# Kernel tuning notes

Hardware: AMD Instinct MI355X
Metric: run time of the kernel (lower is better)

## Reference

```python
import jax, jax.numpy as jnp
import numpy as np

B, F, N, E, T = 8, 16, 1024, 256, 64
ALPHA = 0.2        # LeakyReLU negative slope
NEG = -9.0e15      # masking value used by the torch code


def setup_inputs() -> dict:
    key = jax.random.key(0)
    ks = jax.random.split(key, 9)
    x = jax.random.normal(ks[0], (B, F, N, T), dtype=jnp.float32)
    mask = (jax.random.uniform(ks[1], (B, F, N, T)) > 0.2).astype(jnp.float32)
    # binary incidence matrix [n_nodes, n_edges]; guarantee every hyperedge
    # has at least one incident node (avoids div-by-zero / empty softmax)
    inc = (jax.random.uniform(ks[2], (N, E)) < 0.05).astype(jnp.float32)
    inc = inc.at[0, :].set(1.0)
    h0 = jax.random.normal(ks[3], (1, N), dtype=jnp.float32)      # initial node state row
    h1 = jax.random.normal(ks[4], (E, 1), dtype=jnp.float32)      # initial edge state
    bias = jax.random.uniform(ks[5], (N,), dtype=jnp.float32)     # THGAT.bias (d_model == N)
    weight = jax.random.uniform(ks[6], (2 * F + 1,), dtype=jnp.float32)  # [3*d_in-ish, 1] proj
    weight2 = jax.random.uniform(ks[7], (E, E), dtype=jnp.float32) / E   # edge mixing
    a = jax.random.uniform(ks[8], (2,), dtype=jnp.float32)        # GAT attention vector
    return {"x": x, "mask": mask, "incidence": inc, "h0": h0, "h1": h1,
            "bias": bias, "weight": weight, "weight2": weight2, "a": a}


def _thgat_step(x_s, m_s, n_s, h_e, incidence, bias, weight, weight2, a):
    # x_s, m_s: [B,F,N]; n_s: [B,1,N]; h_e: [B,E,1]
    x_cat = jnp.concatenate([x_s, m_s, n_s], axis=1)          # [B,2F+1,N]
    xn = jnp.einsum('bcn,c->bn', x_cat, weight) + bias         # node feature (scalar per node)
    deg = jnp.sum(incidence, axis=0)                           # [E] hyperedge degree
    edge = (xn @ incidence) / deg                              # [B,E] mean of incident nodes
    edge = edge @ weight2                                      # [B,E]
    # pairwise GAT score at nonzero (n,e) pairs; computed densely then masked,
    # identical math to torch's gather -> sparse_coo -> to_dense path
    s = jax.nn.leaky_relu(xn[:, :, None] * a[0] + edge[:, None, :] * a[1], ALPHA)  # [B,N,E]
    time_e = h_e[:, :, 0] + edge                               # agg_type='sum': pri_e + edge
    s = s + time_e[:, None, :]
    att = jnp.where(incidence[None] > 0, s, NEG)
    attn = jax.nn.softmax(att, axis=1)                         # softmax over nodes per edge
    node = jnp.einsum('bne,be->bn', attn, edge)                # aggregate edge feats to nodes
    return node[:, None, :], edge[:, :, None]                  # [B,1,N], [B,E,1]


def reference(x, mask, incidence, h0, h1, bias, weight, weight2, a):
    n0 = jnp.broadcast_to(h0[None], (B, 1, N))
    e0 = jnp.broadcast_to(h1[None], (B, E, 1))
    xs = jnp.moveaxis(x, -1, 0)     # [T,B,F,N]
    ms = jnp.moveaxis(mask, -1, 0)

    def step(carry, inp):
        n_s, h_e = carry
        x_s, m_s = inp
        node, edge = _thgat_step(x_s, m_s, n_s, h_e, incidence, bias, weight, weight2, a)
        return (node, edge), node[:, 0, :]

    _, nodes = jax.lax.scan(step, (n0, e0), (xs, ms))
    return jnp.moveaxis(nodes, 0, 1)  # [B,T,N] imputations per timestep
```

## Files before the change

### kernel.cpp

```cpp
#include <hip/hip_runtime.h>

#define Bq 8
#define Fq 16
#define Nq 1024
#define Eq 256
#define Tq 64
constexpr float ALPHAq = 0.2f;
constexpr float LOG2Eq = 1.4426950408889634f;
constexpr int NNZCAP = 32768;
constexpr int MAXJE  = 20;
constexpr int NNZW2  = 20480;
constexpr int DUMP0  = NNZW2;
constexpr int WVLTOT = NNZW2 + 1024;

__device__ __forceinline__ float fast_exp2(float x) {
  return __builtin_amdgcn_exp2f(x);
}

__device__ __forceinline__ float qswap1(float x) {
  return __int_as_float(__builtin_amdgcn_mov_dpp(__float_as_int(x), 0xB1, 0xF, 0xF, true));
}
__device__ __forceinline__ float qswap2(float x) {
  return __int_as_float(__builtin_amdgcn_mov_dpp(__float_as_int(x), 0x4E, 0xF, 0xF, true));
}

__global__ __launch_bounds__(256) void k_cntB(const float* __restrict__ inc,
                                              int* __restrict__ gcnt,
                                              int* __restrict__ ncnt) {
  const int i = blockIdx.x, e = threadIdx.x;
  const int base = i * 64;
  int c = 0;
  for (int r = 0; r < 64; ++r) c += (inc[(size_t)(base + r) * Eq + e] > 0.f) ? 1 : 0;
  gcnt[i * Eq + e] = c;
  if (i < 4) {
    const int n = i * 256 + e;
    const float* row = inc + (size_t)n * Eq;
    int cn = 0;
    for (int k = 0; k < Eq; ++k) cn += (row[k] > 0.f) ? 1 : 0;
    ncnt[n] = cn;
  }
}

__global__ __launch_bounds__(1024) void k_prefB(const int* __restrict__ gcnt,
                                                const int* __restrict__ ncnt,
                                                int* __restrict__ g_ptr,
                                                int* __restrict__ goff,
                                                int* __restrict__ tlp,
                                                int* __restrict__ tlp2) {
  __shared__ int tot[Eq];
  __shared__ int sptr[Eq + 1];
  __shared__ int sn[Nq];
  __shared__ int snp[Nq + 1];
  __shared__ int snp2[Nq + 1];
  const int tid = threadIdx.x;
  if (tid < Eq) { int s = 0; for (int i = 0; i < 16; ++i) s += gcnt[i * Eq + tid]; tot[tid] = s; }
  sn[tid] = ncnt[tid];
  __syncthreads();
  if (tid == 0) { int s = 0; for (int j = 0; j < Eq; ++j) { sptr[j] = s; s += tot[j]; } sptr[Eq] = s; }
  if (tid == 1) { int s = 0; for (int i = 0; i < Nq; ++i) { snp[i] = s; s += sn[i]; } snp[Nq] = s; }
  if (tid == 2) { int s = 0; for (int i = 0; i < Nq; ++i) { snp2[i] = s; s += (sn[i] + 3) & ~3; } snp2[Nq] = s; }
  __syncthreads();
  if (tid <= Eq) g_ptr[tid] = sptr[tid];
  tlp[tid] = snp[tid];
  tlp2[tid] = snp2[tid];
  if (tid == 0) { tlp[Nq] = snp[Nq]; tlp2[Nq] = snp2[Nq]; }
  if (tid < Eq) {
    int run = sptr[tid];
    for (int i = 0; i < 16; ++i) { goff[i * Eq + tid] = run; run += gcnt[i * Eq + tid]; }
  }
}

__global__ __launch_bounds__(256) void k_fillB(const float* __restrict__ inc,
                                               const int* __restrict__ goff,
                                               const int* __restrict__ tlp,
                                               unsigned short* __restrict__ g_nodes,
                                               unsigned short* __restrict__ tle_g) {
  const int i = blockIdx.x, e = threadIdx.x;
  const int base = i * 64;
  int w = goff[i * Eq + e];
  for (int r = 0; r < 64; ++r) {
    const int n = base + r;
    if (inc[(size_t)n * Eq + e] > 0.f) { if (w < NNZCAP) g_nodes[w] = (unsigned short)n; ++w; }
  }
  if (i < 4) {
    const int n = i * 256 + e;
    const float* row = inc + (size_t)n * Eq;
    int wn = tlp[n];
    for (int k = 0; k < Eq; ++k)
      if (row[k] > 0.f) { if (wn < NNZCAP) tle_g[wn] = (unsigned short)k; ++wn; }
  }
}

__global__ __launch_bounds__(256) void k_prep(const int* __restrict__ g_ptr,
                                              const unsigned short* __restrict__ g_nodes,
                                              const int* __restrict__ tlp_g,
                                              const int* __restrict__ tlp2_g,
                                              const unsigned short* __restrict__ tle_g,
                                              unsigned* __restrict__ tbl_g,
                                              unsigned short* __restrict__ wpos_g) {
  const int t = blockIdx.x * 256 + threadIdx.x;
  const int e = t >> 2, sub = t & 3;
  const int p0 = g_ptr[e], p1 = g_ptr[e + 1];
  int j = 0;
  for (int pos = p0 + sub; pos < p1; pos += 4, ++j) {
    const int n = (int)g_nodes[pos];
    int lo = tlp_g[n], hi = tlp_g[n + 1];
    while (lo < hi) { int mid = (lo + hi) >> 1; if ((int)tle_g[mid] < e) lo = mid + 1; else hi = mid; }
    int wp = tlp2_g[n] + (lo - tlp_g[n]);
    if (wp >= NNZW2) wp = DUMP0 + t;
    wpos_g[pos] = (unsigned short)wp;
    if (j < MAXJE) tbl_g[j * Nq + t] = ((unsigned)wp << 16) | (unsigned)n;
  }
  for (; j < MAXJE; ++j)
    tbl_g[j * Nq + t] = ((unsigned)(DUMP0 + t) << 16) | (unsigned)Nq;
}

__global__ __launch_bounds__(256) void k_xnp(const float* __restrict__ x,
                                             const float* __restrict__ mask,
                                             const float* __restrict__ weight,
                                             const float* __restrict__ bias,
                                             float* __restrict__ xnpT) {
  __shared__ float accs[64][65];
  const int wg = blockIdx.x;
  const int b = wg >> 4;
  const int n0 = (wg & 15) << 6;
  const int lane = threadIdx.x & 63;
  const int w = threadIdx.x >> 6;
  float a[16];
#pragma unroll
  for (int i = 0; i < 16; ++i) a[i] = 0.f;
  for (int f = 0; f < Fq; ++f) {
    const float wf = weight[f], wm = weight[Fq + f];
#pragma unroll
    for (int ii = 0; ii < 16; ++ii) {
      const int i = w + ii * 4;
      const size_t base = ((size_t)(b * Fq + f) * Nq + n0 + i) * Tq + lane;
      a[ii] += x[base] * wf + mask[base] * wm;
    }
  }
#pragma unroll
  for (int ii = 0; ii < 16; ++ii) accs[w + ii * 4][lane] = a[ii];
  __syncthreads();
  const float bl = bias[n0 + lane];
#pragma unroll
  for (int jj = 0; jj < 16; ++jj) {
    const int tt = w + jj * 4;
    xnpT[((size_t)b * Tq + tt) * Nq + n0 + lane] = accs[lane][tt] + bl;
  }
}

__global__ __attribute__((amdgpu_flat_work_group_size(1024, 1024), amdgpu_waves_per_eu(4, 4)))
void k_recur(
    const float* __restrict__ xnpT, const float* __restrict__ w2,
    const int* __restrict__ g_ptr, const unsigned short* __restrict__ g_nodes,
    const unsigned short* __restrict__ wpos_g,
    const int* __restrict__ tlp_g, const int* __restrict__ tlp2_g,
    const unsigned* __restrict__ tbl_g,
    const float* __restrict__ h0,
    const float* __restrict__ weight, const float* __restrict__ a_vec,
    float* __restrict__ out) {
  __shared__ __align__(16) float wvl[WVLTOT];
  __shared__ float xnl[Nq + 4];
  __shared__ __align__(16) float epp[4 * 72];

  const int b = blockIdx.x;
  const int tid = threadIdx.x;
  const int e = tid >> 2;
  const int sub = tid & 3;
  const float w32 = weight[2 * Fq];
  const float a0 = a_vec[0], a1 = a_vec[1];
  const float a0L = a0 * LOG2Eq;

  for (int i = tid; i < WVLTOT; i += 1024) wvl[i] = 0.f;

  float xn_reg = xnpT[(size_t)b * Tq * Nq + tid] + w32 * h0[tid];
  xnl[tid] = xn_reg;
  if (tid == 0) xnl[Nq] = 0.f;

  unsigned uj[MAXJE];
#pragma unroll
  for (int j = 0; j < MAXJE; ++j) uj[j] = tbl_g[j * Nq + tid];

  float w2r[64];
#pragma unroll
  for (int kk = 0; kk < 64; ++kk)
    w2r[kk] = w2[(size_t)(sub * 64 + kk) * Eq + e];

  const int p0 = g_ptr[e], p1 = g_ptr[e + 1];
  const float degf = (float)(p1 - p0);
  const int tail0 = p0 + sub + 4 * MAXJE;
  const int q0v = tlp2_g[tid] >> 2;
  const int degn = tlp_g[tid + 1] - tlp_g[tid];
  const int iters = (tid == 0) ? 0 : ((degn + 3) >> 2);
  __syncthreads();

  float xv[MAXJE];

  for (int t = 0; t < Tq; ++t) {
    const float xnext = xnpT[((size_t)b * Tq + (t + 1 < Tq ? t + 1 : t)) * Nq + tid];

    float v = 0.f;
    float mxv = -3.0e38f;
#pragma unroll
    for (int j = 0; j < MAXJE; ++j) {
      const int n = (int)(uj[j] & 0xffffu);
      const float xx = xnl[n];
      v += xx;
      const float val = (n < Nq) ? xx : -1.0e30f;
      xv[j] = val;
      mxv = fmaxf(mxv, val);
    }
    for (int pos = tail0; pos < p1; pos += 4) {
      const float xx = xnl[(int)g_nodes[pos]];
      v += xx;
      mxv = fmaxf(mxv, xx);
    }
    v += qswap1(v);
    v += qswap2(v);
    mxv = fmaxf(mxv, qswap1(mxv));
    mxv = fmaxf(mxv, qswap2(mxv));
    if (sub == 0) epp[(e >> 6) * 72 + (e & 63)] = v / degf;
    __syncthreads();

    float acc = 0.f;
#pragma unroll
    for (int k = 0; k < 16; ++k) {
      const float4 epv = *reinterpret_cast<const float4*>(&epp[sub * 72 + (k << 2)]);
      acc += w2r[k * 4 + 0] * epv.x + w2r[k * 4 + 1] * epv.y +
             w2r[k * 4 + 2] * epv.z + w2r[k * 4 + 3] * epv.w;
    }
    acc += qswap1(acc);
    acc += qswap2(acc);
    const float edge2 = acc;
    const float e2a1L = (edge2 * a1) * LOG2Eq;
    const float sm2 = mxv * a0L + e2a1L;
    const float mx2 = fmaxf(sm2, ALPHAq * sm2);

    float Zs = 0.f;
#pragma unroll
    for (int j = 0; j < MAXJE; ++j) {
      const float s2 = xv[j] * a0L + e2a1L;
      const float p = fast_exp2(fmaxf(s2, ALPHAq * s2) - mx2);
      xv[j] = p;
      Zs += p;
    }
    for (int pos = tail0; pos < p1; pos += 4) {
      const float s2 = xnl[(int)g_nodes[pos]] * a0L + e2a1L;
      Zs += fast_exp2(fmaxf(s2, ALPHAq * s2) - mx2);
    }
    Zs += qswap1(Zs);
    Zs += qswap2(Zs);
    const float we = edge2 / Zs;

#pragma unroll
    for (int j = 0; j < MAXJE; ++j)
      wvl[uj[j] >> 16] = xv[j] * we;
    for (int pos = tail0; pos < p1; pos += 4) {
      const float s2 = xnl[(int)g_nodes[pos]] * a0L + e2a1L;
      wvl[(int)wpos_g[pos]] = fast_exp2(fmaxf(s2, ALPHAq * s2) - mx2) * we;
    }
    __syncthreads();

    float nv = 0.f;
    if (tid < 64) {
      const float4 w4 = reinterpret_cast<const float4*>(wvl)[tid];
      float q = w4.x + w4.y + w4.z + w4.w;
#pragma unroll
      for (int m = 32; m > 0; m >>= 1) q += __shfl_xor(q, m);
      if (tid == 0) nv = q;
    }
    for (int i = 0; i < iters; ++i) {
      const float4 w4 = reinterpret_cast<const float4*>(wvl)[q0v + i];
      nv += w4.x + w4.y + w4.z + w4.w;
    }

    out[((size_t)b * Tq + t) * Nq + tid] = nv;
    xn_reg = xnext + w32 * nv;
    xnl[tid] = xn_reg;
    __syncthreads();
  }
}

extern "C" void kernel_launch(void* const* d_in, const int* in_sizes, int n_in,
                              void* d_out, int out_size, void* d_ws, size_t ws_size,
                              hipStream_t stream) {
  (void)in_sizes; (void)n_in; (void)out_size; (void)ws_size;
  const float* x      = (const float*)d_in[0];
  const float* mask   = (const float*)d_in[1];
  const float* inc    = (const float*)d_in[2];
  const float* h0     = (const float*)d_in[3];
  const float* bias   = (const float*)d_in[5];
  const float* weight = (const float*)d_in[6];
  const float* w2     = (const float*)d_in[7];
  const float* avec   = (const float*)d_in[8];
  float* out = (float*)d_out;

  char* ws = (char*)d_ws;
  size_t off = 0;
  auto alloc = [&](size_t bytes) { void* p = ws + off; off += (bytes + 255) & ~(size_t)255; return p; };
  int*            g_ptr   = (int*)alloc((Eq + 1) * 4);
  int*            gcnt    = (int*)alloc(16 * Eq * 4);
  int*            goff    = (int*)alloc(16 * Eq * 4);
  unsigned short* g_nodes = (unsigned short*)alloc((size_t)NNZCAP * 2);
  int*            ncnt    = (int*)alloc(Nq * 4);
  int*            tlp_g   = (int*)alloc((Nq + 1) * 4);
  int*            tlp2_g  = (int*)alloc((Nq + 1) * 4);
  unsigned short* tle_g   = (unsigned short*)alloc((size_t)NNZCAP * 2);
  unsigned short* wpos_g  = (unsigned short*)alloc((size_t)NNZCAP * 2);
  unsigned*       tbl_g   = (unsigned*)alloc((size_t)MAXJE * Nq * 4);
  float*          xnpT    = (float*)alloc((size_t)Bq * Tq * Nq * 4);

  k_cntB <<<16, 256, 0, stream>>>(inc, gcnt, ncnt);
  k_prefB<<<1, 1024, 0, stream>>>(gcnt, ncnt, g_ptr, goff, tlp_g, tlp2_g);
  k_fillB<<<16, 256, 0, stream>>>(inc, goff, tlp_g, g_nodes, tle_g);
  k_prep <<<4, 256, 0, stream>>>(g_ptr, g_nodes, tlp_g, tlp2_g, tle_g, tbl_g, wpos_g);
  k_xnp  <<<128, 256, 0, stream>>>(x, mask, weight, bias, xnpT);
  k_recur<<<Bq, 1024, 0, stream>>>(xnpT, w2, g_ptr, g_nodes, wpos_g, tlp_g, tlp2_g,
                                   tbl_g, h0, weight, avec, out);
}
```

Measured before the change: 538.0 us.

## Parallelize incidence preprocessing: split row counts, tree prefix scans, dense rank table

Row-degree counting now runs on all 16 blocks with four threads per node using float4 loads, instead of 4 blocks with one thread scanning a whole row. The serial single-thread prefix sums become parallel Hillis-Steele scans across 1024 threads. The per-node sorted edge list and its binary search are replaced by a dense byte rank table indexed by (node, edge), so k_prep does a direct lookup. This shortens the serialized setup kernels but adds a 256 KB rank buffer and more block barriers.

```diff
diff --git a/kernel.cpp b/kernel.cpp
--- a/kernel.cpp
+++ b/kernel.cpp
@@ -24,21 +24,44 @@
   return __int_as_float(__builtin_amdgcn_mov_dpp(__float_as_int(x), 0x4E, 0xF, 0xF, true));
 }
 
+__device__ __forceinline__ int scan_excl_1024(int* s, int tid, int val, int* total) {
+  __syncthreads();
+  s[tid] = val;
+  __syncthreads();
+  for (int d = 1; d < 1024; d <<= 1) {
+    int t = s[tid];
+    if (tid >= d) t += s[tid - d];
+    __syncthreads();
+    s[tid] = t;
+    __syncthreads();
+  }
+  *total = s[1023];
+  return s[tid] - val;
+}
+
 __global__ __launch_bounds__(256) void k_cntB(const float* __restrict__ inc,
                                               int* __restrict__ gcnt,
                                               int* __restrict__ ncnt) {
-  const int i = blockIdx.x, e = threadIdx.x;
-  const int base = i * 64;
-  int c = 0;
-  for (int r = 0; r < 64; ++r) c += (inc[(size_t)(base + r) * Eq + e] > 0.f) ? 1 : 0;
-  gcnt[i * Eq + e] = c;
-  if (i < 4) {
-    const int n = i * 256 + e;
-    const float* row = inc + (size_t)n * Eq;
-    int cn = 0;
-    for (int k = 0; k < Eq; ++k) cn += (row[k] > 0.f) ? 1 : 0;
-    ncnt[n] = cn;
-  }
+  __shared__ int cp[64][4];
+  const int i = blockIdx.x, tid = threadIdx.x;
+  {
+    const int e = tid, base = i * 64;
+    int c = 0;
+    for (int r = 0; r < 64; ++r) c += (inc[(size_t)(base + r) * Eq + e] > 0.f) ? 1 : 0;
+    gcnt[i * Eq + e] = c;
+  }
+  const int nl = tid >> 2, kc = tid & 3, n = i * 64 + nl;
+  {
+    const float4* r4 = (const float4*)(inc + (size_t)n * Eq + kc * 64);
+    int c = 0;
+    for (int j = 0; j < 16; ++j) {
+      const float4 v = r4[j];
+      c += (v.x > 0.f) + (v.y > 0.f) + (v.z > 0.f) + (v.w > 0.f);
+    }
+    cp[nl][kc] = c;
+  }
+  __syncthreads();
+  if (kc == 0) ncnt[n] = cp[nl][0] + cp[nl][1] + cp[nl][2] + cp[nl][3];
 }
 
 __global__ __launch_bounds__(1024) void k_prefB(const int* __restrict__ gcnt,
@@ -47,55 +70,67 @@
                                                 int* __restrict__ goff,
                                                 int* __restrict__ tlp,
                                                 int* __restrict__ tlp2) {
-  __shared__ int tot[Eq];
-  __shared__ int sptr[Eq + 1];
-  __shared__ int sn[Nq];
-  __shared__ int snp[Nq + 1];
-  __shared__ int snp2[Nq + 1];
+  __shared__ int s[1024];
   const int tid = threadIdx.x;
-  if (tid < Eq) { int s = 0; for (int i = 0; i < 16; ++i) s += gcnt[i * Eq + tid]; tot[tid] = s; }
-  sn[tid] = ncnt[tid];
-  __syncthreads();
-  if (tid == 0) { int s = 0; for (int j = 0; j < Eq; ++j) { sptr[j] = s; s += tot[j]; } sptr[Eq] = s; }
-  if (tid == 1) { int s = 0; for (int i = 0; i < Nq; ++i) { snp[i] = s; s += sn[i]; } snp[Nq] = s; }
-  if (tid == 2) { int s = 0; for (int i = 0; i < Nq; ++i) { snp2[i] = s; s += (sn[i] + 3) & ~3; } snp2[Nq] = s; }
-  __syncthreads();
-  if (tid <= Eq) g_ptr[tid] = sptr[tid];
-  tlp[tid] = snp[tid];
-  tlp2[tid] = snp2[tid];
-  if (tid == 0) { tlp[Nq] = snp[Nq]; tlp2[Nq] = snp2[Nq]; }
+  int tot;
+  int tote = 0;
+  if (tid < Eq) for (int i = 0; i < 16; ++i) tote += gcnt[i * Eq + tid];
+  const int exE = scan_excl_1024(s, tid, (tid < Eq) ? tote : 0, &tot);
   if (tid < Eq) {
-    int run = sptr[tid];
+    g_ptr[tid] = exE;
+    int run = exE;
     for (int i = 0; i < 16; ++i) { goff[i * Eq + tid] = run; run += gcnt[i * Eq + tid]; }
   }
+  if (tid == 0) g_ptr[Eq] = tot;
+  const int dn = ncnt[tid];
+  const int exN = scan_excl_1024(s, tid, dn, &tot);
+  tlp[tid] = exN;
+  if (tid == 0) tlp[Nq] = tot;
+  const int dp = (dn + 3) & ~3;
+  const int exP = scan_excl_1024(s, tid, dp, &tot);
+  tlp2[tid] = exP;
+  if (tid == 0) tlp2[Nq] = tot;
 }
 
 __global__ __launch_bounds__(256) void k_fillB(const float* __restrict__ inc,
                                                const int* __restrict__ goff,
-                                               const int* __restrict__ tlp,
                                                unsigned short* __restrict__ g_nodes,
-                                               unsigned short* __restrict__ tle_g) {
-  const int i = blockIdx.x, e = threadIdx.x;
-  const int base = i * 64;
-  int w = goff[i * Eq + e];
-  for (int r = 0; r < 64; ++r) {
-    const int n = base + r;
-    if (inc[(size_t)n * Eq + e] > 0.f) { if (w < NNZCAP) g_nodes[w] = (unsigned short)n; ++w; }
-  }
-  if (i < 4) {
-    const int n = i * 256 + e;
-    const float* row = inc + (size_t)n * Eq;
-    int wn = tlp[n];
-    for (int k = 0; k < Eq; ++k)
-      if (row[k] > 0.f) { if (wn < NNZCAP) tle_g[wn] = (unsigned short)k; ++wn; }
+                                               unsigned char* __restrict__ rank8) {
+  __shared__ int cp[64][4];
+  const int i = blockIdx.x, tid = threadIdx.x;
+  {
+    const int e = tid, base = i * 64;
+    int w = goff[i * Eq + e];
+    for (int r = 0; r < 64; ++r) {
+      const int n = base + r;
+      if (inc[(size_t)n * Eq + e] > 0.f) { if (w < NNZCAP) g_nodes[w] = (unsigned short)n; ++w; }
+    }
+  }
+  const int nl = tid >> 2, kc = tid & 3, n = i * 64 + nl;
+  const float* row = inc + (size_t)n * Eq + kc * 64;
+  {
+    const float4* r4 = (const float4*)row;
+    int c = 0;
+    for (int j = 0; j < 16; ++j) {
+      const float4 v = r4[j];
+      c += (v.x > 0.f) + (v.y > 0.f) + (v.z > 0.f) + (v.w > 0.f);
+    }
+    cp[nl][kc] = c;
+  }
+  __syncthreads();
+  {
+    int base = 0;
+    for (int c2 = 0; c2 < kc; ++c2) base += cp[nl][c2];
+    int r = base;
+    for (int k = 0; k < 64; ++k)
+      if (row[k] > 0.f) { rank8[(size_t)n * Eq + kc * 64 + k] = (unsigned char)r; ++r; }
   }
 }
 
 __global__ __launch_bounds__(256) void k_prep(const int* __restrict__ g_ptr,
                                               const unsigned short* __restrict__ g_nodes,
-                                              const int* __restrict__ tlp_g,
                                               const int* __restrict__ tlp2_g,
-                                              const unsigned short* __restrict__ tle_g,
+                                              const unsigned char* __restrict__ rank8,
                                               unsigned* __restrict__ tbl_g,
                                               unsigned short* __restrict__ wpos_g) {
   const int t = blockIdx.x * 256 + threadIdx.x;
@@ -104,9 +139,7 @@
   int j = 0;
   for (int pos = p0 + sub; pos < p1; pos += 4, ++j) {
     const int n = (int)g_nodes[pos];
-    int lo = tlp_g[n], hi = tlp_g[n + 1];
-    while (lo < hi) { int mid = (lo + hi) >> 1; if ((int)tle_g[mid] < e) lo = mid + 1; else hi = mid; }
-    int wp = tlp2_g[n] + (lo - tlp_g[n]);
+    int wp = tlp2_g[n] + (int)rank8[(size_t)n * Eq + e];
     if (wp >= NNZW2) wp = DUMP0 + t;
     wpos_g[pos] = (unsigned short)wp;
     if (j < MAXJE) tbl_g[j * Nq + t] = ((unsigned)wp << 16) | (unsigned)n;
@@ -305,15 +338,15 @@
   int*            ncnt    = (int*)alloc(Nq * 4);
   int*            tlp_g   = (int*)alloc((Nq + 1) * 4);
   int*            tlp2_g  = (int*)alloc((Nq + 1) * 4);
-  unsigned short* tle_g   = (unsigned short*)alloc((size_t)NNZCAP * 2);
+  unsigned char*  rank8   = (unsigned char*)alloc((size_t)Nq * Eq);
   unsigned short* wpos_g  = (unsigned short*)alloc((size_t)NNZCAP * 2);
   unsigned*       tbl_g   = (unsigned*)alloc((size_t)MAXJE * Nq * 4);
   float*          xnpT    = (float*)alloc((size_t)Bq * Tq * Nq * 4);
 
   k_cntB <<<16, 256, 0, stream>>>(inc, gcnt, ncnt);
   k_prefB<<<1, 1024, 0, stream>>>(gcnt, ncnt, g_ptr, goff, tlp_g, tlp2_g);
-  k_fillB<<<16, 256, 0, stream>>>(inc, goff, tlp_g, g_nodes, tle_g);
-  k_prep <<<4, 256, 0, stream>>>(g_ptr, g_nodes, tlp_g, tlp2_g, tle_g, tbl_g, wpos_g);
+  k_fillB<<<16, 256, 0, stream>>>(inc, goff, g_nodes, rank8);
+  k_prep <<<4, 256, 0, stream>>>(g_ptr, g_nodes, tlp2_g, rank8, tbl_g, wpos_g);
   k_xnp  <<<128, 256, 0, stream>>>(x, mask, weight, bias, xnpT);
   k_recur<<<Bq, 1024, 0, stream>>>(xnpT, w2, g_ptr, g_nodes, wpos_g, tlp_g, tlp2_g,
                                    tbl_g, h0, weight, avec, out);
```

After: 467.0 us. 1.15x faster.
